# Optimization experiments

Hardware: AMD Instinct MI355X
Metric: run time of the kernel (lower is better)

Reference implementation:

```python
import jax, jax.numpy as jnp
import numpy as np

PROJ_DIM = 128
CLASS_NUM = 7
QUEUE_SIZE = 150
TEMP = 0.5
EPS = 1e-8


def _l2norm(x):
    # torch F.normalize(dim=1) with eps clamp
    n = jnp.linalg.norm(x, axis=1, keepdims=True)
    return x / jnp.maximum(n, 1e-12)


def setup_inputs() -> dict:
    key = jax.random.key(0)
    k1, k2, k3, k4 = jax.random.split(key, 4)
    B = 65536
    activation = jax.random.normal(k1, (B, PROJ_DIM), dtype=jnp.float32)
    ema_activation = jax.random.normal(k2, (B, PROJ_DIM), dtype=jnp.float32)
    pseudo_label = jax.random.normal(k3, (B, CLASS_NUM), dtype=jnp.float32)
    queue_list = jax.random.normal(k4, (QUEUE_SIZE * CLASS_NUM, PROJ_DIM), dtype=jnp.float32)
    queue_list = _l2norm(queue_list)  # buffer is row-normalized at init
    return {
        "activation": activation,
        "ema_activation": ema_activation,
        "pseudo_label": pseudo_label,
        "queue_list": queue_list,
    }


def reference(activation, ema_activation, pseudo_label, queue_list):
    f = _l2norm(activation)          # [B, D]
    ema_f = _l2norm(ema_activation)  # [B, D]
    label = jnp.argmax(pseudo_label, axis=1)  # [B]

    # positive pair term: exp(<f_i, ema_f_i>/T)
    l_pos = jnp.exp(jnp.sum(f * ema_f, axis=1) / TEMP)  # [B]

    # similarities against the (snapshotted) queue: [B, C*Qs]
    sim = jnp.exp(jnp.einsum("bd,qd->bq", f, queue_list) / TEMP)

    # denominator = l_pos + pos_sum + neg_sum = l_pos + total_sum over queue
    denom = l_pos + jnp.sum(sim, axis=1)  # [B]

    # which queue rows belong to each sample's pseudo-class
    row_class = jnp.arange(CLASS_NUM * QUEUE_SIZE) // QUEUE_SIZE  # [C*Qs]
    pos_mask = (row_class[None, :] == label[:, None])             # [B, C*Qs]

    # -log(contrast) terms: the ema term plus the QUEUE_SIZE positive terms
    term0 = -jnp.log(l_pos / denom + EPS)                          # [B]
    term1 = -jnp.log(sim / denom[:, None] + EPS)                   # [B, C*Qs]
    pos_terms = jnp.sum(jnp.where(pos_mask, term1, 0.0), axis=1)   # [B]

    per_sample = (term0 + pos_terms) / (QUEUE_SIZE + 1)
    return jnp.mean(per_sample)
```

## Files before the change

kernel.cpp:

```cpp
#include <hip/hip_runtime.h>
#include <stdint.h>

#define CLASS_NUM 7
#define QROWS 1050
#define QPAD  1152
#define NPAD  102
#define NGRP  72
#define GPW   18
#define QSUM_OFF (QPAD * 128)
#define PART_OFF 151552
#define NBLK  1024
#define C2L 2.8853900817779268f

typedef float f32x4 __attribute__((ext_vector_type(4)));
typedef long  long2v __attribute__((ext_vector_type(2)));

__device__ __forceinline__ float fexp2(float x) { return __builtin_amdgcn_exp2f(x); }

__device__ __forceinline__ unsigned pk8(float a, float b, float c, float d) {
  int v = __builtin_amdgcn_cvt_pk_fp8_f32(a, b, 0, false);
  v = __builtin_amdgcn_cvt_pk_fp8_f32(c, d, v, true);
  return (unsigned)v;
}

__global__ __launch_bounds__(256) void prep_q8(
    const float* __restrict__ queue, char* __restrict__ ws)
{
  const int b = blockIdx.x, tid = threadIdx.x;
  if (b < NGRP) {
    const int g = b;
    const int lane = tid >> 2, k = tid & 3;
    const int row = g * 16 + (lane & 15);
    const int col = k * 32 + (lane >> 4) * 8;
    uint2 u = {0u, 0u};
    if (row < QROWS) {
      const float4 v0 = *(const float4*)(queue + row * 128 + col);
      const float4 v1 = *(const float4*)(queue + row * 128 + col + 4);
      u.x = pk8(v0.x, v0.y, v0.z, v0.w);
      u.y = pk8(v1.x, v1.y, v1.z, v1.w);
    }
    *(uint2*)(ws + (size_t)g * 2048 + tid * 8) = u;
  } else if (tid < 128) {
    const int c = b - NGRP, d = tid;
    float s = 0.f;
    const float* p = queue + c * 150 * 128 + d;
#pragma unroll 10
    for (int i = 0; i < 150; ++i) s += p[i * 128];
    ((float*)(ws + QSUM_OFF))[c * 128 + d] = s;
  }
}

__global__ __launch_bounds__(256, 2) void pgc_stream(
    const float* __restrict__ act, const float* __restrict__ ema,
    const float* __restrict__ plab, char* __restrict__ ws)
{
  __shared__ __align__(16) char aT[8192];
  __shared__ float s_lpos[64], s_pd[64];
  __shared__ float dnp[4][64];

  const int tid = threadIdx.x, lane = tid & 63, wave = tid >> 6;
  const int lo = lane & 15, hi = lane >> 4;

  {
    const int r = tid >> 2, j4 = tid & 3;
    const long grow = (long)blockIdx.x * 64 + r;
    const float* ap = act + grow * 128 + j4 * 32;
    const float* ep = ema + grow * 128 + j4 * 32;

    float pv0 = plab[grow * CLASS_NUM + j4];
    float pv1 = (j4 + 4 < CLASS_NUM) ? plab[grow * CLASS_NUM + j4 + 4] : -3.4e38f;
    f32x4 a4[8], e4[8];
#pragma unroll
    for (int u = 0; u < 8; ++u) a4[u] = *(const f32x4*)(ap + 4 * u);
#pragma unroll
    for (int u = 0; u < 8; ++u) e4[u] = *(const f32x4*)(ep + 4 * u);

    float a2 = 0.f, e2 = 0.f, ae = 0.f;
#pragma unroll
    for (int u = 0; u < 8; ++u) {
      a2 += a4[u].x*a4[u].x + a4[u].y*a4[u].y + a4[u].z*a4[u].z + a4[u].w*a4[u].w;
      e2 += e4[u].x*e4[u].x + e4[u].y*e4[u].y + e4[u].z*e4[u].z + e4[u].w*e4[u].w;
      ae += a4[u].x*e4[u].x + a4[u].y*e4[u].y + a4[u].z*e4[u].z + a4[u].w*e4[u].w;
    }
#pragma unroll
    for (int m = 1; m < 4; m <<= 1) {
      a2 += __shfl_xor(a2, m);
      e2 += __shfl_xor(e2, m);
      ae += __shfl_xor(ae, m);
    }
    const float rna = rsqrtf(a2), rne = rsqrtf(e2);

    float pv = pv0; int bi = j4;
    if (pv1 > pv0) { pv = pv1; bi = j4 + 4; }
#pragma unroll
    for (int m = 1; m < 4; m <<= 1) {
      const float ov = __shfl_xor(pv, m);
      const int   oi = __shfl_xor(bi, m);
      if (ov > pv || (ov == pv && oi < bi)) { pv = ov; bi = oi; }
    }

    const float* qs = (const float*)(ws + QSUM_OFF) + bi * 128 + j4 * 32;
    float pdot = 0.f;
#pragma unroll
    for (int u = 0; u < 8; ++u) {
      const float4 qv = *(const float4*)(qs + 4 * u);
      pdot += a4[u].x*qv.x + a4[u].y*qv.y + a4[u].z*qv.z + a4[u].w*qv.w;
    }
#pragma unroll
    for (int m = 1; m < 4; m <<= 1) pdot += __shfl_xor(pdot, m);

    if (j4 == 0) {
      s_lpos[r] = ae * rna * rne * C2L;
      s_pd[r]   = pdot * rna;
    }

    const float sc = rna * C2L;
    const int st = r >> 4, lr = r & 15;
#pragma unroll
    for (int cc = 0; cc < 4; ++cc) {
      const f32x4 x = a4[cc * 2], y = a4[cc * 2 + 1];
      uint2 u;
      u.x = pk8(x.x * sc, x.y * sc, x.z * sc, x.w * sc);
      u.y = pk8(y.x * sc, y.y * sc, y.z * sc, y.w * sc);
      *(uint2*)(aT + st * 2048 + (cc * 16 + lr) * 32 + j4 * 8) = u;
    }
  }
  __syncthreads();

  long2v sa[4][2];
#pragma unroll
  for (int s = 0; s < 4; ++s) {
    sa[s][0] = *(const long2v*)(aT + s * 2048 + lane * 32);
    sa[s][1] = *(const long2v*)(aT + s * 2048 + lane * 32 + 16);
  }

  float dn[4][4] = {{0.f,0.f,0.f,0.f},{0.f,0.f,0.f,0.f},
                    {0.f,0.f,0.f,0.f},{0.f,0.f,0.f,0.f}};
  const f32x4 Z = {0.f, 0.f, 0.f, 0.f};
  const char* qp = ws + (size_t)(wave * GPW) * 2048 + (size_t)lane * 32;

  long2v B0a, B0b, B1a, B1b;
#define LOADG(Xa, Xb, G)                                                \
  { Xa = *(const long2v*)(qp + (G) * 2048);                             \
    Xb = *(const long2v*)(qp + (G) * 2048 + 16); }
#define COMPG(Xa, Xb)                                                   \
  { _Pragma("unroll")                                                   \
    for (int s = 0; s < 4; ++s) {                                       \
      f32x4 c = Z;                                                      \
      c = __builtin_amdgcn_mfma_f32_16x16x32_fp8_fp8(sa[s][0][0], Xa[0], c, 0, 0, 0); \
      c = __builtin_amdgcn_mfma_f32_16x16x32_fp8_fp8(sa[s][0][1], Xa[1], c, 0, 0, 0); \
      c = __builtin_amdgcn_mfma_f32_16x16x32_fp8_fp8(sa[s][1][0], Xb[0], c, 0, 0, 0); \
      c = __builtin_amdgcn_mfma_f32_16x16x32_fp8_fp8(sa[s][1][1], Xb[1], c, 0, 0, 0); \
      _Pragma("unroll")                                                 \
      for (int rg = 0; rg < 4; ++rg) dn[s][rg] += fexp2(c[rg]);         \
    } }

  LOADG(B0a, B0b, 0)
  LOADG(B1a, B1b, 1)
#pragma unroll 1
  for (int g = 0; g < GPW - 2; g += 2) {
    COMPG(B0a, B0b) LOADG(B0a, B0b, g + 2)
    COMPG(B1a, B1b) LOADG(B1a, B1b, g + 3)
  }
  COMPG(B0a, B0b)
  COMPG(B1a, B1b)
#undef LOADG
#undef COMPG

#pragma unroll
  for (int s = 0; s < 4; ++s)
#pragma unroll
    for (int rg = 0; rg < 4; ++rg)
#pragma unroll
      for (int m = 1; m < 16; m <<= 1)
        dn[s][rg] += __shfl_xor(dn[s][rg], m);

  if (lo == 0) {
#pragma unroll
    for (int s = 0; s < 4; ++s)
#pragma unroll
      for (int rg = 0; rg < 4; ++rg)
        dnp[wave][s * 16 + hi * 4 + rg] = dn[s][rg];
  }
  __syncthreads();

  if (tid < 64) {
    const int i = tid;
    const float dtot = dnp[0][i] + dnp[1][i] + dnp[2][i] + dnp[3][i];
    const float lp   = exp2f(s_lpos[i]);
    const float dnf  = lp + dtot - (float)NPAD;
    float loss = -logf(lp / dnf + 1e-8f) + 150.0f * logf(dnf) - 2.0f * s_pd[i];
#pragma unroll
    for (int m = 1; m < 64; m <<= 1) loss += __shfl_xor(loss, m);
    if (tid == 0)
      ((float*)(ws + PART_OFF))[blockIdx.x] = loss;
  }
}

__global__ __launch_bounds__(1024) void finalize(
    const char* __restrict__ ws, float* __restrict__ out)
{
  __shared__ float sred[16];
  const int tid = threadIdx.x;
  float v = ((const float*)(ws + PART_OFF))[tid];
#pragma unroll
  for (int m = 1; m < 64; m <<= 1) v += __shfl_xor(v, m);
  if ((tid & 63) == 0) sred[tid >> 6] = v;
  __syncthreads();
  if (tid < 16) {
    float s = sred[tid];
#pragma unroll
    for (int m = 1; m < 16; m <<= 1) s += __shfl_xor(s, m);
    if (tid == 0) *out = s * (1.0f / (151.0f * 65536.0f));
  }
}

extern "C" void kernel_launch(void* const* d_in, const int* in_sizes, int n_in,
                              void* d_out, int out_size, void* d_ws, size_t ws_size,
                              hipStream_t stream) {
  const float* act   = (const float*)d_in[0];
  const float* ema   = (const float*)d_in[1];
  const float* plab  = (const float*)d_in[2];
  const float* queue = (const float*)d_in[3];
  float* out = (float*)d_out;

  prep_q8<<<dim3(NGRP + CLASS_NUM), dim3(256), 0, stream>>>(queue, (char*)d_ws);

  pgc_stream<<<dim3(NBLK), dim3(256), 0, stream>>>(
      act, ema, plab, (char*)d_ws);

  finalize<<<dim3(1), dim3(1024), 0, stream>>>((const char*)d_ws, out);
}
```

Before: 41.58 us.

## Process 128 rows per block to reuse each queue fragment across eight MFMA tiles

Each block now handles 128 samples instead of 64, so every loaded fp8 queue group feeds eight independent MFMA accumulator chains instead of four. The MFMAs are interleaved across the tiles, which hides MFMA latency and halves total queue reads from global/L2. The cost is double the registers and LDS per block, occupancy dropping to one block per SM setting, and only 512 blocks on the device. The prologue uses two threads per row and the final reduction is adjusted to match.

```diff
diff --git a/kernel.cpp b/kernel.cpp
--- a/kernel.cpp
+++ b/kernel.cpp
@@ -9,7 +9,7 @@
 #define GPW   18
 #define QSUM_OFF (QPAD * 128)
 #define PART_OFF 151552
-#define NBLK  1024
+#define NBLK  512
 #define C2L 2.8853900817779268f
 
 typedef float f32x4 __attribute__((ext_vector_type(4)));
@@ -50,66 +50,65 @@
   }
 }
 
-__global__ __launch_bounds__(256, 2) void pgc_stream(
+__global__ __launch_bounds__(256, 1) void pgc_stream(
     const float* __restrict__ act, const float* __restrict__ ema,
     const float* __restrict__ plab, char* __restrict__ ws)
 {
-  __shared__ __align__(16) char aT[8192];
-  __shared__ float s_lpos[64], s_pd[64];
-  __shared__ float dnp[4][64];
+  __shared__ __align__(16) char aT[16384];
+  __shared__ float s_lpos[128], s_pd[128];
+  __shared__ float dnp[4][128];
 
   const int tid = threadIdx.x, lane = tid & 63, wave = tid >> 6;
   const int lo = lane & 15, hi = lane >> 4;
 
   {
-    const int r = tid >> 2, j4 = tid & 3;
-    const long grow = (long)blockIdx.x * 64 + r;
-    const float* ap = act + grow * 128 + j4 * 32;
-    const float* ep = ema + grow * 128 + j4 * 32;
-
-    float pv0 = plab[grow * CLASS_NUM + j4];
-    float pv1 = (j4 + 4 < CLASS_NUM) ? plab[grow * CLASS_NUM + j4 + 4] : -3.4e38f;
-    f32x4 a4[8], e4[8];
-#pragma unroll
-    for (int u = 0; u < 8; ++u) a4[u] = *(const f32x4*)(ap + 4 * u);
-#pragma unroll
-    for (int u = 0; u < 8; ++u) e4[u] = *(const f32x4*)(ep + 4 * u);
+    const int r = tid >> 1, j2 = tid & 1;
+    const long grow = (long)blockIdx.x * 128 + r;
+    const float* ap = act + grow * 128 + j2 * 64;
+    const float* ep = ema + grow * 128 + j2 * 64;
+
+    const float* pp = plab + grow * CLASS_NUM;
+    float pv; int bi;
+    if (j2 == 0) { pv = pp[0]; bi = 0;
+      for (int c = 1; c < 4; ++c) { const float v = pp[c]; if (v > pv) { pv = v; bi = c; } }
+    } else { pv = pp[4]; bi = 4;
+      for (int c = 5; c < 7; ++c) { const float v = pp[c]; if (v > pv) { pv = v; bi = c; } }
+    }
+
+    f32x4 a4[16], e4[16];
+#pragma unroll
+    for (int u = 0; u < 16; ++u) a4[u] = *(const f32x4*)(ap + 4 * u);
+#pragma unroll
+    for (int u = 0; u < 16; ++u) e4[u] = *(const f32x4*)(ep + 4 * u);
 
     float a2 = 0.f, e2 = 0.f, ae = 0.f;
 #pragma unroll
-    for (int u = 0; u < 8; ++u) {
+    for (int u = 0; u < 16; ++u) {
       a2 += a4[u].x*a4[u].x + a4[u].y*a4[u].y + a4[u].z*a4[u].z + a4[u].w*a4[u].w;
       e2 += e4[u].x*e4[u].x + e4[u].y*e4[u].y + e4[u].z*e4[u].z + e4[u].w*e4[u].w;
       ae += a4[u].x*e4[u].x + a4[u].y*e4[u].y + a4[u].z*e4[u].z + a4[u].w*e4[u].w;
     }
-#pragma unroll
-    for (int m = 1; m < 4; m <<= 1) {
-      a2 += __shfl_xor(a2, m);
-      e2 += __shfl_xor(e2, m);
-      ae += __shfl_xor(ae, m);
-    }
+    a2 += __shfl_xor(a2, 1);
+    e2 += __shfl_xor(e2, 1);
+    ae += __shfl_xor(ae, 1);
     const float rna = rsqrtf(a2), rne = rsqrtf(e2);
 
-    float pv = pv0; int bi = j4;
-    if (pv1 > pv0) { pv = pv1; bi = j4 + 4; }
-#pragma unroll
-    for (int m = 1; m < 4; m <<= 1) {
-      const float ov = __shfl_xor(pv, m);
-      const int   oi = __shfl_xor(bi, m);
+    {
+      const float ov = __shfl_xor(pv, 1);
+      const int   oi = __shfl_xor(bi, 1);
       if (ov > pv || (ov == pv && oi < bi)) { pv = ov; bi = oi; }
     }
 
-    const float* qs = (const float*)(ws + QSUM_OFF) + bi * 128 + j4 * 32;
+    const float* qs = (const float*)(ws + QSUM_OFF) + bi * 128 + j2 * 64;
     float pdot = 0.f;
 #pragma unroll
-    for (int u = 0; u < 8; ++u) {
+    for (int u = 0; u < 16; ++u) {
       const float4 qv = *(const float4*)(qs + 4 * u);
       pdot += a4[u].x*qv.x + a4[u].y*qv.y + a4[u].z*qv.z + a4[u].w*qv.w;
     }
-#pragma unroll
-    for (int m = 1; m < 4; m <<= 1) pdot += __shfl_xor(pdot, m);
-
-    if (j4 == 0) {
+    pdot += __shfl_xor(pdot, 1);
+
+    if (j2 == 0) {
       s_lpos[r] = ae * rna * rne * C2L;
       s_pd[r]   = pdot * rna;
     }
@@ -117,25 +116,30 @@
     const float sc = rna * C2L;
     const int st = r >> 4, lr = r & 15;
 #pragma unroll
-    for (int cc = 0; cc < 4; ++cc) {
-      const f32x4 x = a4[cc * 2], y = a4[cc * 2 + 1];
+    for (int cc8 = 0; cc8 < 8; ++cc8) {
+      const int k = j2 * 2 + (cc8 >> 2), hi_ = cc8 & 3;
+      const f32x4 x = a4[2 * cc8], y = a4[2 * cc8 + 1];
       uint2 u;
       u.x = pk8(x.x * sc, x.y * sc, x.z * sc, x.w * sc);
       u.y = pk8(y.x * sc, y.y * sc, y.z * sc, y.w * sc);
-      *(uint2*)(aT + st * 2048 + (cc * 16 + lr) * 32 + j4 * 8) = u;
-    }
-  }
-  __syncthreads();
-
-  long2v sa[4][2];
-#pragma unroll
-  for (int s = 0; s < 4; ++s) {
+      *(uint2*)(aT + st * 2048 + (hi_ * 16 + lr) * 32 + k * 8) = u;
+    }
+  }
+  __syncthreads();
+
+  long2v sa[8][2];
+#pragma unroll
+  for (int s = 0; s < 8; ++s) {
     sa[s][0] = *(const long2v*)(aT + s * 2048 + lane * 32);
     sa[s][1] = *(const long2v*)(aT + s * 2048 + lane * 32 + 16);
   }
 
-  float dn[4][4] = {{0.f,0.f,0.f,0.f},{0.f,0.f,0.f,0.f},
-                    {0.f,0.f,0.f,0.f},{0.f,0.f,0.f,0.f}};
+  float dn[8][4];
+#pragma unroll
+  for (int s = 0; s < 8; ++s)
+#pragma unroll
+    for (int rg = 0; rg < 4; ++rg) dn[s][rg] = 0.f;
+
   const f32x4 Z = {0.f, 0.f, 0.f, 0.f};
   const char* qp = ws + (size_t)(wave * GPW) * 2048 + (size_t)lane * 32;
 
@@ -144,16 +148,26 @@
   { Xa = *(const long2v*)(qp + (G) * 2048);                             \
     Xb = *(const long2v*)(qp + (G) * 2048 + 16); }
 #define COMPG(Xa, Xb)                                                   \
-  { _Pragma("unroll")                                                   \
-    for (int s = 0; s < 4; ++s) {                                       \
-      f32x4 c = Z;                                                      \
-      c = __builtin_amdgcn_mfma_f32_16x16x32_fp8_fp8(sa[s][0][0], Xa[0], c, 0, 0, 0); \
-      c = __builtin_amdgcn_mfma_f32_16x16x32_fp8_fp8(sa[s][0][1], Xa[1], c, 0, 0, 0); \
-      c = __builtin_amdgcn_mfma_f32_16x16x32_fp8_fp8(sa[s][1][0], Xb[0], c, 0, 0, 0); \
-      c = __builtin_amdgcn_mfma_f32_16x16x32_fp8_fp8(sa[s][1][1], Xb[1], c, 0, 0, 0); \
+  { f32x4 c[8];                                                         \
+    _Pragma("unroll")                                                   \
+    for (int s = 0; s < 8; ++s) c[s] = Z;                               \
+    _Pragma("unroll")                                                   \
+    for (int s = 0; s < 8; ++s)                                         \
+      c[s] = __builtin_amdgcn_mfma_f32_16x16x32_fp8_fp8(sa[s][0][0], Xa[0], c[s], 0, 0, 0); \
+    _Pragma("unroll")                                                   \
+    for (int s = 0; s < 8; ++s)                                         \
+      c[s] = __builtin_amdgcn_mfma_f32_16x16x32_fp8_fp8(sa[s][0][1], Xa[1], c[s], 0, 0, 0); \
+    _Pragma("unroll")                                                   \
+    for (int s = 0; s < 8; ++s)                                         \
+      c[s] = __builtin_amdgcn_mfma_f32_16x16x32_fp8_fp8(sa[s][1][0], Xb[0], c[s], 0, 0, 0); \
+    _Pragma("unroll")                                                   \
+    for (int s = 0; s < 8; ++s)                                         \
+      c[s] = __builtin_amdgcn_mfma_f32_16x16x32_fp8_fp8(sa[s][1][1], Xb[1], c[s], 0, 0, 0); \
+    _Pragma("unroll")                                                   \
+    for (int s = 0; s < 8; ++s)                                         \
       _Pragma("unroll")                                                 \
-      for (int rg = 0; rg < 4; ++rg) dn[s][rg] += fexp2(c[rg]);         \
-    } }
+      for (int rg = 0; rg < 4; ++rg) dn[s][rg] += fexp2(c[s][rg]);      \
+  }
 
   LOADG(B0a, B0b, 0)
   LOADG(B1a, B1b, 1)
@@ -168,7 +182,7 @@
 #undef COMPG
 
 #pragma unroll
-  for (int s = 0; s < 4; ++s)
+  for (int s = 0; s < 8; ++s)
 #pragma unroll
     for (int rg = 0; rg < 4; ++rg)
 #pragma unroll
@@ -177,40 +191,43 @@
 
   if (lo == 0) {
 #pragma unroll
-    for (int s = 0; s < 4; ++s)
+    for (int s = 0; s < 8; ++s)
 #pragma unroll
       for (int rg = 0; rg < 4; ++rg)
         dnp[wave][s * 16 + hi * 4 + rg] = dn[s][rg];
   }
   __syncthreads();
 
-  if (tid < 64) {
+  float loss = 0.f;
+  if (tid < 128) {
     const int i = tid;
     const float dtot = dnp[0][i] + dnp[1][i] + dnp[2][i] + dnp[3][i];
     const float lp   = exp2f(s_lpos[i]);
     const float dnf  = lp + dtot - (float)NPAD;
-    float loss = -logf(lp / dnf + 1e-8f) + 150.0f * logf(dnf) - 2.0f * s_pd[i];
-#pragma unroll
-    for (int m = 1; m < 64; m <<= 1) loss += __shfl_xor(loss, m);
-    if (tid == 0)
-      ((float*)(ws + PART_OFF))[blockIdx.x] = loss;
-  }
-}
-
-__global__ __launch_bounds__(1024) void finalize(
+    loss = -logf(lp / dnf + 1e-8f) + 150.0f * logf(dnf) - 2.0f * s_pd[i];
+  }
+#pragma unroll
+  for (int m = 1; m < 64; m <<= 1) loss += __shfl_xor(loss, m);
+  if (lane == 0) dnp[0][wave] = loss;
+  __syncthreads();
+  if (tid == 0)
+    ((float*)(ws + PART_OFF))[blockIdx.x] = dnp[0][0] + dnp[0][1];
+
+}
+__global__ __launch_bounds__(512) void finalize(
     const char* __restrict__ ws, float* __restrict__ out)
 {
-  __shared__ float sred[16];
+  __shared__ float sred[8];
   const int tid = threadIdx.x;
   float v = ((const float*)(ws + PART_OFF))[tid];
 #pragma unroll
   for (int m = 1; m < 64; m <<= 1) v += __shfl_xor(v, m);
   if ((tid & 63) == 0) sred[tid >> 6] = v;
   __syncthreads();
-  if (tid < 16) {
+  if (tid < 8) {
     float s = sred[tid];
 #pragma unroll
-    for (int m = 1; m < 16; m <<= 1) s += __shfl_xor(s, m);
+    for (int m = 1; m < 8; m <<= 1) s += __shfl_xor(s, m);
     if (tid == 0) *out = s * (1.0f / (151.0f * 65536.0f));
   }
 }
@@ -226,8 +243,7 @@
 
   prep_q8<<<dim3(NGRP + CLASS_NUM), dim3(256), 0, stream>>>(queue, (char*)d_ws);
 
-  pgc_stream<<<dim3(NBLK), dim3(256), 0, stream>>>(
-      act, ema, plab, (char*)d_ws);
-
-  finalize<<<dim3(1), dim3(1024), 0, stream>>>((const char*)d_ws, out);
-}
+  pgc_stream<<<dim3(NBLK), dim3(256), 0, stream>>>(act, ema, plab, (char*)d_ws);
+
+  finalize<<<dim3(1), dim3(512), 0, stream>>>((const char*)d_ws, out);
+}
```

Measured after the change: 51.24 us. +23.2%, slower.
